# Kernel optimization log

Measured on AMD Instinct MI355X. Metric: run time of the kernel, lower is better.

Reference implementation:

```python
import jax, jax.numpy as jnp
import numpy as np

EPS = 1e-6

def _ln(x, g, b):
    mu = jnp.mean(x, -1, keepdims=True)
    var = jnp.mean((x - mu) ** 2, -1, keepdims=True)
    return (x - mu) / jnp.sqrt(var + EPS) * g + b

def _attn(q, k, v, nh, mask=None):
    B, Lq, H = q.shape
    Lk = k.shape[1]
    dh = H // nh
    q = q.reshape(B, Lq, nh, dh).transpose(0, 2, 1, 3)
    k = k.reshape(B, Lk, nh, dh).transpose(0, 2, 1, 3)
    v = v.reshape(B, Lk, nh, dh).transpose(0, 2, 1, 3)
    s = jnp.einsum('bhqd,bhkd->bhqk', q, k) * (1.0 / np.float32(np.sqrt(dh)))
    if mask is not None:
        s = jnp.where(mask, jnp.float32(-1e30), s)
    a = jax.nn.softmax(s, axis=-1)
    o = jnp.einsum('bhqk,bhkd->bhqd', a, v)
    return o.transpose(0, 2, 1, 3).reshape(B, Lq, H)

def _forward(byte_seq, patch_boundaries, emb, g_ln1_g, g_ln1_b, g_wqkv, g_bqkv, g_wo, g_bo,
             g_ln2_g, g_ln2_b, g_w1, g_b1, g_w2, g_b2, fn_g, fn_b,
             ca_ln_g, ca_ln_b, ca_wqkv, ca_bqkv, ca_wo, ca_bo, head_w, head_b,
             n_heads=16, ca_heads=8):
    B, S = byte_seq.shape
    P = patch_boundaries.shape[1]
    H = emb.shape[1]
    x = emb[byte_seq]  # [B,S,H] byte embeddings (local encoder)
    # ragged patch pooling: patch id of byte i = #boundaries <= i (BabylonIndex patches)
    pos = jnp.arange(S)
    pid = jax.vmap(lambda bd: jnp.searchsorted(bd, pos, side='right'))(patch_boundaries)
    pid = jnp.clip(pid, 0, P - 1)
    seg = lambda vals, ids: jax.ops.segment_sum(vals, ids, num_segments=P)
    sums = jax.vmap(seg)(x, pid)                                  # [B,P,H]
    cnts = jax.vmap(seg)(jnp.ones((B, S), x.dtype), pid)          # [B,P]
    patches = sums / jnp.maximum(cnts, 1.0)[..., None]            # mean-pooled patch reps
    causal = jnp.triu(jnp.ones((P, P), bool), 1)
    def layer(h, p):
        l1g, l1b, wqkv, bqkv, wo, bo, l2g, l2b, w1, b1, w2, b2 = p
        n = _ln(h, l1g, l1b)
        q, k, v = jnp.split(n @ wqkv + bqkv, 3, axis=-1)
        h = h + _attn(q, k, v, n_heads, causal) @ wo + bo
        n2 = _ln(h, l2g, l2b)
        h = h + jax.nn.gelu(n2 @ w1 + b1, approximate=False) @ w2 + b2
        return h, None
    patches, _ = jax.lax.scan(layer, patches, (g_ln1_g, g_ln1_b, g_wqkv, g_bqkv, g_wo, g_bo,
                                               g_ln2_g, g_ln2_b, g_w1, g_b1, g_w2, g_b2))
    patches = _ln(patches, fn_g, fn_b)  # GlobalLatentTransformer.final_norm
    # cross attention: byte queries attend to global patch representations
    qn = _ln(x, ca_ln_g, ca_ln_b)
    kvn = _ln(patches, ca_ln_g, ca_ln_b)
    q = qn @ ca_wqkv[:, :H] + ca_bqkv[:H]
    k = kvn @ ca_wqkv[:, H:2 * H] + ca_bqkv[H:2 * H]
    v = kvn @ ca_wqkv[:, 2 * H:] + ca_bqkv[2 * H:]
    h = x + _attn(q, k, v, ca_heads) @ ca_wo + ca_bo
    return h @ head_w + head_b  # [B,S,256] next-byte logits

def setup_inputs() -> dict:
    key = jax.random.key(0)
    ks = jax.random.split(key, 16)
    B, S, P, H, L, V = 2, 4096, 256, 1024, 4, 256
    std = 0.02
    d = {}
    d['byte_seq'] = jax.random.randint(ks[0], (B, S), 0, V, dtype=jnp.int32)
    d['patch_boundaries'] = jnp.sort(jax.random.randint(ks[1], (B, P), 1, S, dtype=jnp.int32), axis=-1)
    d['emb'] = jax.random.normal(ks[2], (V, H), jnp.float32) * std
    d['g_ln1_g'] = jnp.ones((L, H), jnp.float32)
    d['g_ln1_b'] = jnp.zeros((L, H), jnp.float32)
    d['g_wqkv'] = jax.random.normal(ks[3], (L, H, 3 * H), jnp.float32) * std
    d['g_bqkv'] = jnp.zeros((L, 3 * H), jnp.float32)
    d['g_wo'] = jax.random.normal(ks[4], (L, H, H), jnp.float32) * std
    d['g_bo'] = jnp.zeros((L, H), jnp.float32)
    d['g_ln2_g'] = jnp.ones((L, H), jnp.float32)
    d['g_ln2_b'] = jnp.zeros((L, H), jnp.float32)
    d['g_w1'] = jax.random.normal(ks[5], (L, H, 4 * H), jnp.float32) * std
    d['g_b1'] = jnp.zeros((L, 4 * H), jnp.float32)
    d['g_w2'] = jax.random.normal(ks[6], (L, 4 * H, H), jnp.float32) * std
    d['g_b2'] = jnp.zeros((L, H), jnp.float32)
    d['fn_g'] = jnp.ones((H,), jnp.float32)
    d['fn_b'] = jnp.zeros((H,), jnp.float32)
    d['ca_ln_g'] = jnp.ones((H,), jnp.float32)
    d['ca_ln_b'] = jnp.zeros((H,), jnp.float32)
    d['ca_wqkv'] = jax.random.normal(ks[7], (H, 3 * H), jnp.float32) * std
    d['ca_bqkv'] = jnp.zeros((3 * H,), jnp.float32)
    d['ca_wo'] = jax.random.normal(ks[8], (H, H), jnp.float32) * std
    d['ca_bo'] = jnp.zeros((H,), jnp.float32)
    d['head_w'] = jax.random.normal(ks[9], (H, V), jnp.float32) * std
    d['head_b'] = jnp.zeros((V,), jnp.float32)
    return d

def reference(byte_seq, patch_boundaries, emb, g_ln1_g, g_ln1_b, g_wqkv, g_bqkv, g_wo, g_bo,
              g_ln2_g, g_ln2_b, g_w1, g_b1, g_w2, g_b2, fn_g, fn_b,
              ca_ln_g, ca_ln_b, ca_wqkv, ca_bqkv, ca_wo, ca_bo, head_w, head_b):
    return _forward(byte_seq, patch_boundaries, emb, g_ln1_g, g_ln1_b, g_wqkv, g_bqkv, g_wo, g_bo,
                    g_ln2_g, g_ln2_b, g_w1, g_b1, g_w2, g_b2, fn_g, fn_b,
                    ca_ln_g, ca_ln_b, ca_wqkv, ca_bqkv, ca_wo, ca_bo, head_w, head_b)
```

## Files before the change

kernel.cpp:

```cpp
#include <hip/hip_runtime.h>
#include <hip/hip_bf16.h>
#include <math.h>

#define Hdim 1024
#define Bsz  2
#define Slen 4096
#define Pn   256
#define NLAY 4

typedef __attribute__((ext_vector_type(8))) __bf16 bfrag;
typedef __attribute__((ext_vector_type(4))) float  f32x4;

__device__ __forceinline__ float gelu_exact(float x) {
  return 0.5f * x * (1.0f + erff(x * 0.70710678118654752f));
}
__device__ __forceinline__ short f2b(float x) {
  __hip_bfloat16 h = __float2bfloat16(x);
  return *reinterpret_cast<short*>(&h);
}
__device__ __forceinline__ void gload16(const short* g, short* l) {
  __builtin_amdgcn_global_load_lds(
      (const __attribute__((address_space(1))) unsigned int*)g,
      (__attribute__((address_space(3))) unsigned int*)l, 16, 0, 0);
}
__device__ __forceinline__ void xcd_remap(int& bx, int& by) {
  int nwg = gridDim.x * gridDim.y;
  int bid = blockIdx.y * gridDim.x + blockIdx.x;
  int wg = (bid & 7) * (nwg >> 3) + (bid >> 3);
  bx = wg % gridDim.x;
  by = wg / gridDim.x;
}

__global__ void embed_ln_kernel(const int* __restrict__ seq, const float* __restrict__ emb,
                                const float* __restrict__ g, const float* __restrict__ bvec,
                                float* __restrict__ x, short* __restrict__ qn) {
  int row = blockIdx.x;
  int tid = threadIdx.x;
  int tok = seq[row];
  float4 v = *(const float4*)(emb + (size_t)tok * Hdim + tid * 4);
  *(float4*)(x + (size_t)row * Hdim + tid * 4) = v;
  float s  = v.x + v.y + v.z + v.w;
  float ss = v.x * v.x + v.y * v.y + v.z * v.z + v.w * v.w;
#pragma unroll
  for (int off = 32; off; off >>= 1) { s += __shfl_xor(s, off); ss += __shfl_xor(ss, off); }
  __shared__ float rs[4], rss[4];
  int wid = tid >> 6;
  if ((tid & 63) == 0) { rs[wid] = s; rss[wid] = ss; }
  __syncthreads();
  float tot  = rs[0] + rs[1] + rs[2] + rs[3];
  float tot2 = rss[0] + rss[1] + rss[2] + rss[3];
  float mu = tot * (1.0f / Hdim);
  float var = tot2 * (1.0f / Hdim) - mu * mu;
  float rstd = rsqrtf(var + 1e-6f);
  float4 gg = *(const float4*)(g + tid * 4);
  float4 bb = *(const float4*)(bvec + tid * 4);
  short4 o;
  o.x = f2b((v.x - mu) * rstd * gg.x + bb.x);
  o.y = f2b((v.y - mu) * rstd * gg.y + bb.y);
  o.z = f2b((v.z - mu) * rstd * gg.z + bb.z);
  o.w = f2b((v.w - mu) * rstd * gg.w + bb.w);
  *(short4*)(qn + (size_t)row * Hdim + tid * 4) = o;
}

__global__ void pid_kernel(const int* __restrict__ bounds, int* __restrict__ pid) {
  int i = blockIdx.x * 256 + threadIdx.x;
  int b = i >> 12;
  int s = i & (Slen - 1);
  const int* bd = bounds + b * Pn;
  int lo = 0, hi = Pn;
  while (lo < hi) { int m = (lo + hi) >> 1; if (bd[m] <= s) lo = m + 1; else hi = m; }
  pid[i] = min(lo, Pn - 1);
}

__global__ void pool_kernel(const float* __restrict__ x, const int* __restrict__ pid,
                            float* __restrict__ patches) {
  int bp = blockIdx.x;
  int b = bp >> 8;
  int p = bp & (Pn - 1);
  const int* pv = pid + b * Slen;
  int lo = 0, hi = Slen;
  while (lo < hi) { int m = (lo + hi) >> 1; if (pv[m] < p) lo = m + 1; else hi = m; }
  int start = lo;
  lo = 0; hi = Slen;
  while (lo < hi) { int m = (lo + hi) >> 1; if (pv[m] < p + 1) lo = m + 1; else hi = m; }
  int end = lo;
  int tid = threadIdx.x;
  float4 acc = {0.f, 0.f, 0.f, 0.f};
  for (int s = start; s < end; ++s) {
    float4 xv = *(const float4*)(x + ((size_t)(b * Slen + s)) * Hdim + tid * 4);
    acc.x += xv.x; acc.y += xv.y; acc.z += xv.z; acc.w += xv.w;
  }
  float cnt = (float)(end - start);
  float r = 1.0f / fmaxf(cnt, 1.0f);
  float4 o = {acc.x * r, acc.y * r, acc.z * r, acc.w * r};
  *(float4*)(patches + (size_t)bp * Hdim + tid * 4) = o;
}

template<int OBF>
__global__ void ln_kernel(const float* __restrict__ in, const float* __restrict__ g,
                          const float* __restrict__ bvec, void* __restrict__ outv) {
  int row = blockIdx.x;
  int tid = threadIdx.x;
  const float* xr = in + (size_t)row * Hdim;
  float4 v = *(const float4*)(xr + tid * 4);
  float s  = v.x + v.y + v.z + v.w;
  float ss = v.x * v.x + v.y * v.y + v.z * v.z + v.w * v.w;
#pragma unroll
  for (int off = 32; off; off >>= 1) { s += __shfl_xor(s, off); ss += __shfl_xor(ss, off); }
  __shared__ float rs[4], rss[4];
  int wid = tid >> 6;
  if ((tid & 63) == 0) { rs[wid] = s; rss[wid] = ss; }
  __syncthreads();
  float tot  = rs[0] + rs[1] + rs[2] + rs[3];
  float tot2 = rss[0] + rss[1] + rss[2] + rss[3];
  float mu = tot * (1.0f / Hdim);
  float var = tot2 * (1.0f / Hdim) - mu * mu;
  float rstd = rsqrtf(var + 1e-6f);
  float4 gg = *(const float4*)(g + tid * 4);
  float4 bb = *(const float4*)(bvec + tid * 4);
  float4 r;
  r.x = (v.x - mu) * rstd * gg.x + bb.x;
  r.y = (v.y - mu) * rstd * gg.y + bb.y;
  r.z = (v.z - mu) * rstd * gg.z + bb.z;
  r.w = (v.w - mu) * rstd * gg.w + bb.w;
  if (OBF) {
    short4 o; o.x = f2b(r.x); o.y = f2b(r.y); o.z = f2b(r.z); o.w = f2b(r.w);
    *(short4*)((short*)outv + (size_t)row * Hdim + tid * 4) = o;
  } else {
    *(float4*)((float*)outv + (size_t)row * Hdim + tid * 4) = r;
  }
}

__global__ void wconv_kernel(const float* __restrict__ in, short* __restrict__ out,
                             int ldin, int K, size_t in_lstride, size_t out_lstride) {
  int z = blockIdx.z;
  const float* src = in + (size_t)z * in_lstride;
  short* dst = out + (size_t)z * out_lstride;
  int n0 = blockIdx.x * 32, k0 = blockIdx.y * 32;
  int tx = threadIdx.x & 31, ty = threadIdx.x >> 5;
  __shared__ float t[32][33];
#pragma unroll
  for (int i = 0; i < 4; i++)
    t[ty + 8 * i][tx] = src[(size_t)(k0 + ty + 8 * i) * ldin + n0 + tx];
  __syncthreads();
#pragma unroll
  for (int i = 0; i < 4; i++)
    dst[(size_t)(n0 + ty + 8 * i) * K + k0 + tx] = f2b(t[tx][ty + 8 * i]);
}

__global__ void vt_kernel(const float* __restrict__ in, short* __restrict__ out) {
  int bh = blockIdx.z; int h = bh & 7; int b = bh >> 3;
  int kk0 = blockIdx.x * 32, d0 = blockIdx.y * 32;
  int tx = threadIdx.x & 31, ty = threadIdx.x >> 5;
  __shared__ float t[32][33];
  const float* src = in + (size_t)b * Pn * Hdim + h * 128;
#pragma unroll
  for (int i = 0; i < 4; i++)
    t[ty + 8 * i][tx] = src[(size_t)(kk0 + ty + 8 * i) * Hdim + d0 + tx];
  __syncthreads();
  short* dst = out + (size_t)bh * 128 * 256;
#pragma unroll
  for (int i = 0; i < 4; i++)
    dst[(size_t)(d0 + ty + 8 * i) * 256 + kk0 + tx] = f2b(t[tx][ty + 8 * i]);
}

__global__ void vtg_kernel(const short* __restrict__ qkvb, short* __restrict__ out) {
  int bh = blockIdx.z; int h = bh & 15; int b = bh >> 4;
  int kk0 = blockIdx.x * 32, d0 = blockIdx.y * 32;
  int tx = threadIdx.x & 31, ty = threadIdx.x >> 5;
  __shared__ short t[32][33];
  const short* src = qkvb + (size_t)b * Pn * 3072 + 2048 + h * 64;
#pragma unroll
  for (int i = 0; i < 4; i++)
    t[ty + 8 * i][tx] = src[(size_t)(kk0 + ty + 8 * i) * 3072 + d0 + tx];
  __syncthreads();
  short* dst = out + (size_t)bh * 64 * 256;
#pragma unroll
  for (int i = 0; i < 4; i++)
    dst[(size_t)(d0 + ty + 8 * i) * 256 + kk0 + tx] = t[tx][ty + 8 * i];
}

template<int EPI, int OBF, int SWZ>
__launch_bounds__(256)
__global__ void gemm_bf16(const short* __restrict__ A, const short* __restrict__ Bt,
                          const float* __restrict__ bias, const float* __restrict__ res,
                          void* __restrict__ Cv, int ldc, int K) {
  __shared__ short As[2][128 * 64];
  __shared__ short Bs[2][128 * 64];
  int tid = threadIdx.x;
  int bx = blockIdx.x, by = blockIdx.y;
  if (SWZ) xcd_remap(bx, by);
  int n0 = bx * 128, m0 = by * 128;
  int lr = tid >> 3;
  int lc = (((tid & 7) ^ (lr & 7)) * 8);
  int wid = tid >> 6, lane = tid & 63;
  int wm = (wid & 1) * 64, wn = (wid >> 1) * 64;
  int quad = lane >> 4, l16 = lane & 15;
  f32x4 acc[4][4];
#pragma unroll
  for (int i = 0; i < 4; i++)
#pragma unroll
    for (int j = 0; j < 4; j++) acc[i][j] = (f32x4){0.f, 0.f, 0.f, 0.f};

  const short* ga = A + (size_t)(m0 + lr) * K + lc;
  const short* gb = Bt + (size_t)(n0 + lr) * K + lc;
  short* la = &As[0][tid * 8];
  short* lb = &Bs[0][tid * 8];

#pragma unroll
  for (int r = 0; r < 4; r++) {
    gload16(ga + (size_t)(r * 32) * K, la + r * 2048);
    gload16(gb + (size_t)(r * 32) * K, lb + r * 2048);
  }
  asm volatile("s_waitcnt vmcnt(0)" ::: "memory");
  __builtin_amdgcn_s_barrier();

  int NT = K >> 6;
  for (int t = 0; t < NT; ++t) {
    int cur = t & 1;
    if (t + 1 < NT) {
      int nb = (cur ^ 1) * 8192;
      int k1 = (t + 1) << 6;
#pragma unroll
      for (int r = 0; r < 4; r++) {
        gload16(ga + (size_t)(r * 32) * K + k1, la + nb + r * 2048);
        gload16(gb + (size_t)(r * 32) * K + k1, lb + nb + r * 2048);
      }
    }
#pragma unroll
    for (int kk = 0; kk < 2; kk++) {
      bfrag af[4], bfv[4];
#pragma unroll
      for (int mi = 0; mi < 4; mi++) {
        int row = wm + mi * 16 + l16;
        af[mi] = *reinterpret_cast<const bfrag*>(
            &As[cur][row * 64 + (((kk * 4 + quad) ^ (row & 7)) * 8)]);
      }
#pragma unroll
      for (int ni = 0; ni < 4; ni++) {
        int row = wn + ni * 16 + l16;
        bfv[ni] = *reinterpret_cast<const bfrag*>(
            &Bs[cur][row * 64 + (((kk * 4 + quad) ^ (row & 7)) * 8)]);
      }
#pragma unroll
      for (int mi = 0; mi < 4; mi++)
#pragma unroll
        for (int ni = 0; ni < 4; ni++)
          acc[mi][ni] = __builtin_amdgcn_mfma_f32_16x16x32_bf16(af[mi], bfv[ni], acc[mi][ni], 0, 0, 0);
    }
    asm volatile("s_waitcnt vmcnt(0)" ::: "memory");
    __builtin_amdgcn_s_barrier();
  }

#pragma unroll
  for (int mi = 0; mi < 4; mi++)
#pragma unroll
    for (int ni = 0; ni < 4; ni++) {
      int c = n0 + wn + ni * 16 + l16;
      float bsv = bias[c];
#pragma unroll
      for (int reg = 0; reg < 4; reg++) {
        int r = m0 + wm + mi * 16 + quad * 4 + reg;
        float v = acc[mi][ni][reg] + bsv;
        if (EPI == 1) v = gelu_exact(v);
        if (EPI == 2) v += res[(size_t)r * ldc + c];
        if (OBF) ((short*)Cv)[(size_t)r * ldc + c] = f2b(v);
        else     ((float*)Cv)[(size_t)r * ldc + c] = v;
      }
    }
}

template<int EPI, int OBF, int SWZ>
__launch_bounds__(256)
__global__ void gemm_bf16_64(const short* __restrict__ A, const short* __restrict__ Bt,
                             const float* __restrict__ bias, const float* __restrict__ res,
                             void* __restrict__ Cv, int ldc, int K) {
  __shared__ short As[2][64 * 64];
  __shared__ short Bs[2][64 * 64];
  int tid = threadIdx.x;
  int bx = blockIdx.x, by = blockIdx.y;
  if (SWZ) xcd_remap(bx, by);
  int n0 = bx * 64, m0 = by * 64;
  int lr = tid >> 3;
  int lc = (((tid & 7) ^ (lr & 7)) * 8);
  int wid = tid >> 6, lane = tid & 63;
  int wm = (wid & 1) * 32, wn = (wid >> 1) * 32;
  int quad = lane >> 4, l16 = lane & 15;
  f32x4 acc[2][2];
#pragma unroll
  for (int i = 0; i < 2; i++)
#pragma unroll
    for (int j = 0; j < 2; j++) acc[i][j] = (f32x4){0.f, 0.f, 0.f, 0.f};

  const short* ga = A + (size_t)(m0 + lr) * K + lc;
  const short* gb = Bt + (size_t)(n0 + lr) * K + lc;
  short* la = &As[0][tid * 8];
  short* lb = &Bs[0][tid * 8];

#pragma unroll
  for (int r = 0; r < 2; r++) {
    gload16(ga + (size_t)(r * 32) * K, la + r * 2048);
    gload16(gb + (size_t)(r * 32) * K, lb + r * 2048);
  }
  asm volatile("s_waitcnt vmcnt(0)" ::: "memory");
  __builtin_amdgcn_s_barrier();

  int NT = K >> 6;
  for (int t = 0; t < NT; ++t) {
    int cur = t & 1;
    if (t + 1 < NT) {
      int nb = (cur ^ 1) * 4096;
      int k1 = (t + 1) << 6;
#pragma unroll
      for (int r = 0; r < 2; r++) {
        gload16(ga + (size_t)(r * 32) * K + k1, la + nb + r * 2048);
        gload16(gb + (size_t)(r * 32) * K + k1, lb + nb + r * 2048);
      }
    }
#pragma unroll
    for (int kk = 0; kk < 2; kk++) {
      bfrag af[2], bfv[2];
#pragma unroll
      for (int mi = 0; mi < 2; mi++) {
        int row = wm + mi * 16 + l16;
        af[mi] = *reinterpret_cast<const bfrag*>(
            &As[cur][row * 64 + (((kk * 4 + quad) ^ (row & 7)) * 8)]);
      }
#pragma unroll
      for (int ni = 0; ni < 2; ni++) {
        int row = wn + ni * 16 + l16;
        bfv[ni] = *reinterpret_cast<const bfrag*>(
            &Bs[cur][row * 64 + (((kk * 4 + quad) ^ (row & 7)) * 8)]);
      }
#pragma unroll
      for (int mi = 0; mi < 2; mi++)
#pragma unroll
        for (int ni = 0; ni < 2; ni++)
          acc[mi][ni] = __builtin_amdgcn_mfma_f32_16x16x32_bf16(af[mi], bfv[ni], acc[mi][ni], 0, 0, 0);
    }
    asm volatile("s_waitcnt vmcnt(0)" ::: "memory");
    __builtin_amdgcn_s_barrier();
  }

#pragma unroll
  for (int mi = 0; mi < 2; mi++)
#pragma unroll
    for (int ni = 0; ni < 2; ni++) {
      int c = n0 + wn + ni * 16 + l16;
      float bsv = bias[c];
#pragma unroll
      for (int reg = 0; reg < 4; reg++) {
        int r = m0 + wm + mi * 16 + quad * 4 + reg;
        float v = acc[mi][ni][reg] + bsv;
        if (EPI == 1) v = gelu_exact(v);
        if (EPI == 2) v += res[(size_t)r * ldc + c];
        if (OBF) ((short*)Cv)[(size_t)r * ldc + c] = f2b(v);
        else     ((float*)Cv)[(size_t)r * ldc + c] = v;
      }
    }
}

__launch_bounds__(256)
__global__ void gemm_splitk(const short* __restrict__ A, const short* __restrict__ Bt,
                            float* __restrict__ part, int K, int Ks) {
  __shared__ short As[2][64 * 64];
  __shared__ short Bs[2][64 * 64];
  int tid = threadIdx.x;
  int n0 = blockIdx.x * 64, m0 = blockIdx.y * 64, s = blockIdx.z;
  int kbase = s * Ks;
  int lr = tid >> 3;
  int lc = (((tid & 7) ^ (lr & 7)) * 8);
  int wid = tid >> 6, lane = tid & 63;
  int wm = (wid & 1) * 32, wn = (wid >> 1) * 32;
  int quad = lane >> 4, l16 = lane & 15;
  f32x4 acc[2][2];
#pragma unroll
  for (int i = 0; i < 2; i++)
#pragma unroll
    for (int j = 0; j < 2; j++) acc[i][j] = (f32x4){0.f, 0.f, 0.f, 0.f};

  const short* ga = A + (size_t)(m0 + lr) * K + kbase + lc;
  const short* gb = Bt + (size_t)(n0 + lr) * K + kbase + lc;
  short* la = &As[0][tid * 8];
  short* lb = &Bs[0][tid * 8];

#pragma unroll
  for (int r = 0; r < 2; r++) {
    gload16(ga + (size_t)(r * 32) * K, la + r * 2048);
    gload16(gb + (size_t)(r * 32) * K, lb + r * 2048);
  }
  asm volatile("s_waitcnt vmcnt(0)" ::: "memory");
  __builtin_amdgcn_s_barrier();

  int NT = Ks >> 6;
  for (int t = 0; t < NT; ++t) {
    int cur = t & 1;
    if (t + 1 < NT) {
      int nb = (cur ^ 1) * 4096;
      int k1 = (t + 1) << 6;
#pragma unroll
      for (int r = 0; r < 2; r++) {
        gload16(ga + (size_t)(r * 32) * K + k1, la + nb + r * 2048);
        gload16(gb + (size_t)(r * 32) * K + k1, lb + nb + r * 2048);
      }
    }
#pragma unroll
    for (int kk = 0; kk < 2; kk++) {
      bfrag af[2], bfv[2];
#pragma unroll
      for (int mi = 0; mi < 2; mi++) {
        int row = wm + mi * 16 + l16;
        af[mi] = *reinterpret_cast<const bfrag*>(
            &As[cur][row * 64 + (((kk * 4 + quad) ^ (row & 7)) * 8)]);
      }
#pragma unroll
      for (int ni = 0; ni < 2; ni++) {
        int row = wn + ni * 16 + l16;
        bfv[ni] = *reinterpret_cast<const bfrag*>(
            &Bs[cur][row * 64 + (((kk * 4 + quad) ^ (row & 7)) * 8)]);
      }
#pragma unroll
      for (int mi = 0; mi < 2; mi++)
#pragma unroll
        for (int ni = 0; ni < 2; ni++)
          acc[mi][ni] = __builtin_amdgcn_mfma_f32_16x16x32_bf16(af[mi], bfv[ni], acc[mi][ni], 0, 0, 0);
    }
    asm volatile("s_waitcnt vmcnt(0)" ::: "memory");
    __builtin_amdgcn_s_barrier();
  }

#pragma unroll
  for (int mi = 0; mi < 2; mi++)
#pragma unroll
    for (int ni = 0; ni < 2; ni++) {
      int c = n0 + wn + ni * 16 + l16;
#pragma unroll
      for (int reg = 0; reg < 4; reg++) {
        int r = m0 + wm + mi * 16 + quad * 4 + reg;
        part[(size_t)s * 524288 + (size_t)r * 1024 + c] = acc[mi][ni][reg];
      }
    }
}

__global__ void w2red_kernel(const float* __restrict__ part, const float* __restrict__ bias,
                             float* __restrict__ patches) {
  int i = (blockIdx.x * 256 + threadIdx.x) * 4;
  float4 v = *(const float4*)(part + i);
#pragma unroll
  for (int s = 1; s < 4; s++) {
    float4 p = *(const float4*)(part + (size_t)s * 524288 + i);
    v.x += p.x; v.y += p.y; v.z += p.z; v.w += p.w;
  }
  int c = i & 1023;
  float4 bv = *(const float4*)(bias + c);
  float4 rv = *(const float4*)(patches + i);
  v.x += bv.x + rv.x; v.y += bv.y + rv.y; v.z += bv.z + rv.z; v.w += bv.w + rv.w;
  *(float4*)(patches + i) = v;
}

__launch_bounds__(256)
__global__ void attn_global3(const short* __restrict__ qkvb, const short* __restrict__ vtg,
                             short* __restrict__ outp) {
  int qt = blockIdx.x;
  int bh = blockIdx.y; int h = bh & 15, b = bh >> 4;
  int tid = threadIdx.x;
  int wid = tid >> 6, lane = tid & 63;
  int quad = lane >> 4, l16 = lane & 15;
  int q0 = qt * 64 + wid * 16;
  __shared__ short KV[64 * 72];
  __shared__ short Pl[4][16][264];
  const short* qrow = qkvb + ((size_t)(b * Pn + q0 + l16)) * 3072 + h * 64 + quad * 8;
  bfrag qf[2];
#pragma unroll
  for (int kd = 0; kd < 2; kd++) qf[kd] = *(const bfrag*)(qrow + kd * 32);
  f32x4 sacc[16];
#pragma unroll
  for (int n = 0; n < 16; n++) sacc[n] = (f32x4){0.f, 0.f, 0.f, 0.f};
  int cr = tid >> 2, cc = (tid & 3) * 16;
#pragma unroll
  for (int kc = 0; kc < 4; kc++) {
    if (kc <= qt) {
      const short* ksrc = qkvb + ((size_t)(b * Pn + kc * 64 + cr)) * 3072 + 1024 + h * 64 + cc;
      int4 v0 = *(const int4*)(ksrc);
      int4 v1 = *(const int4*)(ksrc + 8);
      __syncthreads();
      *(int4*)&KV[cr * 72 + cc] = v0;
      *(int4*)&KV[cr * 72 + cc + 8] = v1;
      __syncthreads();
#pragma unroll
      for (int n = 0; n < 4; n++)
#pragma unroll
        for (int kd = 0; kd < 2; kd++) {
          bfrag kf = *(const bfrag*)&KV[(n * 16 + l16) * 72 + kd * 32 + quad * 8];
          sacc[kc * 4 + n] = __builtin_amdgcn_mfma_f32_16x16x32_bf16(qf[kd], kf, sacc[kc * 4 + n], 0, 0, 0);
        }
    }
  }
  int nfr = (qt + 1) * 4;
  const float scale = 0.125f;
  float mx[4] = {-1e30f, -1e30f, -1e30f, -1e30f};
#pragma unroll
  for (int n = 0; n < 16; n++) {
    if (n < nfr) {
      int col = n * 16 + l16;
#pragma unroll
      for (int r = 0; r < 4; r++)
        if (col <= q0 + quad * 4 + r) mx[r] = fmaxf(mx[r], sacc[n][r]);
    }
  }
#pragma unroll
  for (int off = 1; off < 16; off <<= 1)
#pragma unroll
    for (int r = 0; r < 4; r++) mx[r] = fmaxf(mx[r], __shfl_xor(mx[r], off));
  float ls[4] = {0.f, 0.f, 0.f, 0.f};
#pragma unroll
  for (int n = 0; n < 16; n++) {
    if (n < nfr) {
      int col = n * 16 + l16;
#pragma unroll
      for (int r = 0; r < 4; r++) {
        float p = (col <= q0 + quad * 4 + r) ? __expf((sacc[n][r] - mx[r]) * scale) : 0.f;
        Pl[wid][quad * 4 + r][col] = f2b(p);
        ls[r] += p;
      }
    }
  }
#pragma unroll
  for (int off = 1; off < 16; off <<= 1)
#pragma unroll
    for (int r = 0; r < 4; r++) ls[r] += __shfl_xor(ls[r], off);
  float rl[4];
#pragma unroll
  for (int r = 0; r < 4; r++) rl[r] = 1.0f / ls[r];

  f32x4 oacc[4];
#pragma unroll
  for (int n = 0; n < 4; n++) oacc[n] = (f32x4){0.f, 0.f, 0.f, 0.f};
#pragma unroll
  for (int kc = 0; kc < 4; kc++) {
    if (kc <= qt) {
      const short* vsrc = vtg + (size_t)bh * 64 * 256 + cr * 256 + kc * 64 + cc;
      int4 v0 = *(const int4*)(vsrc);
      int4 v1 = *(const int4*)(vsrc + 8);
      __syncthreads();
      *(int4*)&KV[cr * 72 + cc] = v0;
      *(int4*)&KV[cr * 72 + cc + 8] = v1;
      __syncthreads();
#pragma unroll
      for (int kk = 0; kk < 2; kk++) {
        bfrag pa = *(const bfrag*)&Pl[wid][l16][kc * 64 + kk * 32 + quad * 8];
#pragma unroll
        for (int n = 0; n < 4; n++) {
          bfrag vf = *(const bfrag*)&KV[(n * 16 + l16) * 72 + kk * 32 + quad * 8];
          oacc[n] = __builtin_amdgcn_mfma_f32_16x16x32_bf16(pa, vf, oacc[n], 0, 0, 0);
        }
      }
    }
  }
#pragma unroll
  for (int n = 0; n < 4; n++)
#pragma unroll
    for (int r = 0; r < 4; r++)
      outp[(size_t)(b * Pn + q0 + quad * 4 + r) * Hdim + h * 64 + n * 16 + l16] = f2b(oacc[n][r] * rl[r]);
}

__launch_bounds__(256)
__global__ void attn_cross4(const short* __restrict__ q, const short* __restrict__ k,
                            const short* __restrict__ vt, short* __restrict__ outp) {
  int bh = blockIdx.y; int h = bh & 7, b = bh >> 3;
  int tid = threadIdx.x;
  int wid = tid >> 6, lane = tid & 63;
  int quad = lane >> 4, l16 = lane & 15;
  int q0 = blockIdx.x * 64 + wid * 16;
  __shared__ short KV[9216];
  __shared__ short Pl[4][16][264];
  const short* qrow = q + ((size_t)(b * Slen + q0 + l16)) * Hdim + h * 128 + quad * 8;
  bfrag qf[4];
#pragma unroll
  for (int kd = 0; kd < 4; kd++) qf[kd] = *(const bfrag*)(qrow + kd * 32);
  f32x4 sacc[16];
#pragma unroll
  for (int n = 0; n < 16; n++) sacc[n] = (f32x4){0.f, 0.f, 0.f, 0.f};

  int cr4 = tid >> 2, cc4 = (tid & 3) * 32;
#pragma unroll
  for (int kc = 0; kc < 4; kc++) {
    const short* ksrc = k + ((size_t)(b * Pn + kc * 64 + cr4)) * Hdim + h * 128 + cc4;
    int4 v0 = *(const int4*)(ksrc);
    int4 v1 = *(const int4*)(ksrc + 8);
    int4 v2 = *(const int4*)(ksrc + 16);
    int4 v3 = *(const int4*)(ksrc + 24);
    __syncthreads();
    *(int4*)&KV[cr4 * 136 + cc4]      = v0;
    *(int4*)&KV[cr4 * 136 + cc4 + 8]  = v1;
    *(int4*)&KV[cr4 * 136 + cc4 + 16] = v2;
    *(int4*)&KV[cr4 * 136 + cc4 + 24] = v3;
    __syncthreads();
#pragma unroll
    for (int n = 0; n < 4; n++)
#pragma unroll
      for (int kd = 0; kd < 4; kd++) {
        bfrag kf = *(const bfrag*)&KV[(n * 16 + l16) * 136 + kd * 32 + quad * 8];
        sacc[kc * 4 + n] = __builtin_amdgcn_mfma_f32_16x16x32_bf16(qf[kd], kf, sacc[kc * 4 + n], 0, 0, 0);
      }
  }

  const float scale = 0.088388347648318447f;
  float mx[4] = {-1e30f, -1e30f, -1e30f, -1e30f};
#pragma unroll
  for (int n = 0; n < 16; n++)
#pragma unroll
    for (int r = 0; r < 4; r++) mx[r] = fmaxf(mx[r], sacc[n][r]);
#pragma unroll
  for (int off = 1; off < 16; off <<= 1)
#pragma unroll
    for (int r = 0; r < 4; r++) mx[r] = fmaxf(mx[r], __shfl_xor(mx[r], off));
  float ls[4] = {0.f, 0.f, 0.f, 0.f};
#pragma unroll
  for (int n = 0; n < 16; n++)
#pragma unroll
    for (int r = 0; r < 4; r++) {
      float p = __expf((sacc[n][r] - mx[r]) * scale);
      Pl[wid][quad * 4 + r][n * 16 + l16] = f2b(p);
      ls[r] += p;
    }
#pragma unroll
  for (int off = 1; off < 16; off <<= 1)
#pragma unroll
    for (int r = 0; r < 4; r++) ls[r] += __shfl_xor(ls[r], off);
  float rl[4];
#pragma unroll
  for (int r = 0; r < 4; r++) rl[r] = 1.0f / ls[r];

  f32x4 oacc[8];
#pragma unroll
  for (int n = 0; n < 8; n++) oacc[n] = (f32x4){0.f, 0.f, 0.f, 0.f};
  int cr2 = tid >> 1, cc2 = (tid & 1) * 32;
#pragma unroll
  for (int kc = 0; kc < 4; kc++) {
    const short* vsrc = vt + (size_t)bh * 32768 + cr2 * 256 + kc * 64 + cc2;
    int4 v0 = *(const int4*)(vsrc);
    int4 v1 = *(const int4*)(vsrc + 8);
    int4 v2 = *(const int4*)(vsrc + 16);
    int4 v3 = *(const int4*)(vsrc + 24);
    __syncthreads();
    *(int4*)&KV[cr2 * 72 + cc2]      = v0;
    *(int4*)&KV[cr2 * 72 + cc2 + 8]  = v1;
    *(int4*)&KV[cr2 * 72 + cc2 + 16] = v2;
    *(int4*)&KV[cr2 * 72 + cc2 + 24] = v3;
    __syncthreads();
#pragma unroll
    for (int kk = 0; kk < 2; kk++) {
      bfrag pa = *(const bfrag*)&Pl[wid][l16][kc * 64 + kk * 32 + quad * 8];
#pragma unroll
      for (int n = 0; n < 8; n++) {
        bfrag vf = *(const bfrag*)&KV[(n * 16 + l16) * 72 + kk * 32 + quad * 8];
        oacc[n] = __builtin_amdgcn_mfma_f32_16x16x32_bf16(pa, vf, oacc[n], 0, 0, 0);
      }
    }
  }
#pragma unroll
  for (int n = 0; n < 8; n++)
#pragma unroll
    for (int r = 0; r < 4; r++)
      outp[(size_t)(b * Slen + q0 + quad * 4 + r) * Hdim + h * 128 + n * 16 + l16] = f2b(oacc[n][r] * rl[r]);
}

extern "C" void kernel_launch(void* const* d_in, const int* in_sizes, int n_in,
                              void* d_out, int out_size, void* d_ws, size_t ws_size,
                              hipStream_t stream) {
  const int*   byte_seq = (const int*)d_in[0];
  const int*   pbound   = (const int*)d_in[1];
  const float* emb      = (const float*)d_in[2];
  const float* g_ln1_g  = (const float*)d_in[3];
  const float* g_ln1_b  = (const float*)d_in[4];
  const float* g_wqkv   = (const float*)d_in[5];
  const float* g_bqkv   = (const float*)d_in[6];
  const float* g_wo     = (const float*)d_in[7];
  const float* g_bo     = (const float*)d_in[8];
  const float* g_ln2_g  = (const float*)d_in[9];
  const float* g_ln2_b  = (const float*)d_in[10];
  const float* g_w1     = (const float*)d_in[11];
  const float* g_b1     = (const float*)d_in[12];
  const float* g_w2     = (const float*)d_in[13];
  const float* g_b2     = (const float*)d_in[14];
  const float* fn_g     = (const float*)d_in[15];
  const float* fn_b     = (const float*)d_in[16];
  const float* ca_ln_g  = (const float*)d_in[17];
  const float* ca_ln_b  = (const float*)d_in[18];
  const float* ca_wqkv  = (const float*)d_in[19];
  const float* ca_bqkv  = (const float*)d_in[20];
  const float* ca_wo    = (const float*)d_in[21];
  const float* ca_bo    = (const float*)d_in[22];
  const float* head_w   = (const float*)d_in[23];
  const float* head_b   = (const float*)d_in[24];
  float* out = (float*)d_out;

  float* x       = (float*)d_ws;
  float* patches = x + 8388608;
  float* vbuf    = patches + 524288;
  float* w2part  = vbuf + 524288;
  int*   pid     = (int*)(w2part + 2097152);
  short* nbuf    = (short*)(pid + 8192);
  short* attn_o  = nbuf + 524288;
  short* mid     = attn_o + 524288;
  short* qn      = mid + 2097152;
  short* qb      = qn + 8388608;
  short* xb      = qb + 8388608;
  short* kb      = xb + 8388608;
  short* vt      = kb + 524288;
  short* qkvb    = vt + 524288;
  short* vtg     = qkvb + 1572864;
  short* wqkv_t  = vtg + 524288;
  short* wo_t    = wqkv_t + 12582912;
  short* w1_t    = wo_t + 4194304;
  short* w2_t    = w1_t + 16777216;
  short* caq_t   = w2_t + 16777216;
  short* cak_t   = caq_t + 1048576;
  short* cav_t   = cak_t + 1048576;
  short* cawo_t  = cav_t + 1048576;
  short* head_t  = cawo_t + 1048576;
  short* caout   = qn;

  embed_ln_kernel<<<Bsz * Slen, 256, 0, stream>>>(byte_seq, emb, ca_ln_g, ca_ln_b, x, qn);
  pid_kernel<<<(Bsz * Slen) / 256, 256, 0, stream>>>(pbound, pid);
  pool_kernel<<<Bsz * Pn, 256, 0, stream>>>(x, pid, patches);

  wconv_kernel<<<dim3(96, 32, 4), 256, 0, stream>>>(g_wqkv, wqkv_t, 3072, 1024, 3145728, 3145728);
  wconv_kernel<<<dim3(32, 32, 4), 256, 0, stream>>>(g_wo, wo_t, 1024, 1024, 1048576, 1048576);
  wconv_kernel<<<dim3(128, 32, 4), 256, 0, stream>>>(g_w1, w1_t, 4096, 1024, 4194304, 4194304);
  wconv_kernel<<<dim3(32, 128, 4), 256, 0, stream>>>(g_w2, w2_t, 1024, 4096, 4194304, 4194304);
  wconv_kernel<<<dim3(32, 32, 3), 256, 0, stream>>>(ca_wqkv, caq_t, 3072, 1024, 1024, 1048576);
  wconv_kernel<<<dim3(32, 32, 1), 256, 0, stream>>>(ca_wo, cawo_t, 1024, 1024, 0, 0);
  wconv_kernel<<<dim3(8, 32, 1), 256, 0, stream>>>(head_w, head_t, 256, 1024, 0, 0);

  for (int l = 0; l < NLAY; ++l) {
    ln_kernel<1><<<Bsz * Pn, 256, 0, stream>>>(patches, g_ln1_g + l * Hdim, g_ln1_b + l * Hdim, nbuf);
    gemm_bf16_64<0, 1, 0><<<dim3(48, 8), 256, 0, stream>>>(
        nbuf, wqkv_t + (size_t)l * 3145728, g_bqkv + l * 3072, nullptr, qkvb, 3072, 1024);
    vtg_kernel<<<dim3(8, 2, 32), 256, 0, stream>>>(qkvb, vtg);
    attn_global3<<<dim3(4, 32), 256, 0, stream>>>(qkvb, vtg, attn_o);
    gemm_bf16_64<2, 0, 0><<<dim3(16, 8), 256, 0, stream>>>(
        attn_o, wo_t + (size_t)l * 1048576, g_bo + l * Hdim, patches, patches, 1024, 1024);
    ln_kernel<1><<<Bsz * Pn, 256, 0, stream>>>(patches, g_ln2_g + l * Hdim, g_ln2_b + l * Hdim, nbuf);
    gemm_bf16_64<1, 1, 0><<<dim3(64, 8), 256, 0, stream>>>(
        nbuf, w1_t + (size_t)l * 4194304, g_b1 + l * 4096, nullptr, mid, 4096, 1024);
    gemm_splitk<<<dim3(16, 8, 4), 256, 0, stream>>>(
        mid, w2_t + (size_t)l * 4194304, w2part, 4096, 1024);
    w2red_kernel<<<512, 256, 0, stream>>>(w2part, g_b2 + l * Hdim, patches);
  }

  ln_kernel<0><<<Bsz * Pn, 256, 0, stream>>>(patches, fn_g, fn_b, patches);
  ln_kernel<1><<<Bsz * Pn, 256, 0, stream>>>(patches, ca_ln_g, ca_ln_b, nbuf);

  gemm_bf16_64<0, 1, 0><<<dim3(16, 8), 256, 0, stream>>>(
      nbuf, cak_t, ca_bqkv + 1024, nullptr, kb, 1024, 1024);
  gemm_bf16_64<0, 0, 0><<<dim3(16, 8), 256, 0, stream>>>(
      nbuf, cav_t, ca_bqkv + 2048, nullptr, vbuf, 1024, 1024);
  vt_kernel<<<dim3(8, 4, 16), 256, 0, stream>>>(vbuf, vt);

  gemm_bf16<0, 1, 1><<<dim3(8, 64), 256, 0, stream>>>(
      qn, caq_t, ca_bqkv, nullptr, qb, 1024, 1024);

  attn_cross4<<<dim3(64, 16), 256, 0, stream>>>(qb, kb, vt, caout);

  gemm_bf16<2, 1, 1><<<dim3(8, 64), 256, 0, stream>>>(
      caout, cawo_t, ca_bo, x, xb, 1024, 1024);

  gemm_bf16_64<0, 0, 1><<<dim3(4, 128), 256, 0, stream>>>(
      xb, head_t, head_b, nullptr, out, 256, 1024);
}
```

Before: 771.5 us.

## Double-buffer cross-attention K/V staging with async global-to-LDS loads and XOR swizzle

Rewrites the cross-attention kernel's K and V staging. It now uses direct global-to-LDS loads into two buffers, so the next chunk loads while MFMAs run on the current one, and the V prefetch overlaps the softmax. Padded LDS rows are replaced by an XOR swizzle to avoid bank conflicts, and half the __syncthreads pairs become single barriers with explicit vmcnt waits. The price is more complex synchronisation that depends on the waitcnt ordering being correct. Only this one kernel out of many in the forward pass is affected.

```diff
diff --git a/kernel.cpp b/kernel.cpp
--- a/kernel.cpp
+++ b/kernel.cpp
@@ -565,44 +565,74 @@
 }
 
 __launch_bounds__(256)
-__global__ void attn_cross4(const short* __restrict__ q, const short* __restrict__ k,
+__global__ void attn_cross5(const short* __restrict__ q, const short* __restrict__ k,
                             const short* __restrict__ vt, short* __restrict__ outp) {
   int bh = blockIdx.y; int h = bh & 7, b = bh >> 3;
   int tid = threadIdx.x;
   int wid = tid >> 6, lane = tid & 63;
   int quad = lane >> 4, l16 = lane & 15;
   int q0 = blockIdx.x * 64 + wid * 16;
-  __shared__ short KV[9216];
+  __shared__ short KV[2][8192];
   __shared__ short Pl[4][16][264];
+
   const short* qrow = q + ((size_t)(b * Slen + q0 + l16)) * Hdim + h * 128 + quad * 8;
   bfrag qf[4];
 #pragma unroll
   for (int kd = 0; kd < 4; kd++) qf[kd] = *(const bfrag*)(qrow + kd * 32);
+
+  const short* kbase = k + (size_t)(b * Pn) * Hdim + h * 128;
+  const short* vbase = vt + (size_t)bh * 32768;
+  int krow = tid >> 4;
+  int vrow = tid >> 3;
+  int swzK = (tid & 15) ^ (krow & 7);
+  int swzV = (tid & 7) ^ (vrow & 7);
+  int s3 = l16 & 7;
+
   f32x4 sacc[16];
 #pragma unroll
   for (int n = 0; n < 16; n++) sacc[n] = (f32x4){0.f, 0.f, 0.f, 0.f};
 
-  int cr4 = tid >> 2, cc4 = (tid & 3) * 32;
+  {
+    const short* src = kbase + (size_t)krow * Hdim + swzK * 8;
+    short* dst = &KV[0][tid * 8];
+#pragma unroll
+    for (int r = 0; r < 4; r++)
+      gload16(src + (size_t)(r * 16) * Hdim, dst + r * 2048);
+  }
+  asm volatile("s_waitcnt vmcnt(0)" ::: "memory");
+  __builtin_amdgcn_s_barrier();
+
 #pragma unroll
   for (int kc = 0; kc < 4; kc++) {
-    const short* ksrc = k + ((size_t)(b * Pn + kc * 64 + cr4)) * Hdim + h * 128 + cc4;
-    int4 v0 = *(const int4*)(ksrc);
-    int4 v1 = *(const int4*)(ksrc + 8);
-    int4 v2 = *(const int4*)(ksrc + 16);
-    int4 v3 = *(const int4*)(ksrc + 24);
-    __syncthreads();
-    *(int4*)&KV[cr4 * 136 + cc4]      = v0;
-    *(int4*)&KV[cr4 * 136 + cc4 + 8]  = v1;
-    *(int4*)&KV[cr4 * 136 + cc4 + 16] = v2;
-    *(int4*)&KV[cr4 * 136 + cc4 + 24] = v3;
-    __syncthreads();
-#pragma unroll
-    for (int n = 0; n < 4; n++)
+    if (kc < 3) {
+      const short* src = kbase + (size_t)((kc + 1) * 64 + krow) * Hdim + swzK * 8;
+      short* dst = &KV[(kc + 1) & 1][tid * 8];
+#pragma unroll
+      for (int r = 0; r < 4; r++)
+        gload16(src + (size_t)(r * 16) * Hdim, dst + r * 2048);
+    }
+    const short* kv = KV[kc & 1];
+#pragma unroll
+    for (int n = 0; n < 4; n++) {
+      int roff = (n * 16 + l16) * 128;
 #pragma unroll
       for (int kd = 0; kd < 4; kd++) {
-        bfrag kf = *(const bfrag*)&KV[(n * 16 + l16) * 136 + kd * 32 + quad * 8];
+        bfrag kf = *(const bfrag*)&kv[roff + (((kd * 4 + quad) ^ s3) * 8)];
         sacc[kc * 4 + n] = __builtin_amdgcn_mfma_f32_16x16x32_bf16(qf[kd], kf, sacc[kc * 4 + n], 0, 0, 0);
       }
+    }
+    asm volatile("s_waitcnt vmcnt(0)" ::: "memory");
+    __builtin_amdgcn_s_barrier();
+  }
+
+  {
+    const short* src0 = vbase + (size_t)vrow * 256 + swzV * 8;
+    const short* src1 = src0 + 64;
+#pragma unroll
+    for (int r = 0; r < 4; r++) {
+      gload16(src0 + (size_t)(r * 32) * 256, &KV[0][tid * 8 + r * 2048]);
+      gload16(src1 + (size_t)(r * 32) * 256, &KV[1][tid * 8 + r * 2048]);
+    }
   }
 
   const float scale = 0.088388347648318447f;
@@ -632,33 +662,51 @@
 #pragma unroll
   for (int r = 0; r < 4; r++) rl[r] = 1.0f / ls[r];
 
+  asm volatile("s_waitcnt vmcnt(0)" ::: "memory");
+  __builtin_amdgcn_s_barrier();
+
   f32x4 oacc[8];
 #pragma unroll
   for (int n = 0; n < 8; n++) oacc[n] = (f32x4){0.f, 0.f, 0.f, 0.f};
-  int cr2 = tid >> 1, cc2 = (tid & 1) * 32;
-#pragma unroll
-  for (int kc = 0; kc < 4; kc++) {
-    const short* vsrc = vt + (size_t)bh * 32768 + cr2 * 256 + kc * 64 + cc2;
-    int4 v0 = *(const int4*)(vsrc);
-    int4 v1 = *(const int4*)(vsrc + 8);
-    int4 v2 = *(const int4*)(vsrc + 16);
-    int4 v3 = *(const int4*)(vsrc + 24);
-    __syncthreads();
-    *(int4*)&KV[cr2 * 72 + cc2]      = v0;
-    *(int4*)&KV[cr2 * 72 + cc2 + 8]  = v1;
-    *(int4*)&KV[cr2 * 72 + cc2 + 16] = v2;
-    *(int4*)&KV[cr2 * 72 + cc2 + 24] = v3;
-    __syncthreads();
-#pragma unroll
-    for (int kk = 0; kk < 2; kk++) {
-      bfrag pa = *(const bfrag*)&Pl[wid][l16][kc * 64 + kk * 32 + quad * 8];
-#pragma unroll
-      for (int n = 0; n < 8; n++) {
-        bfrag vf = *(const bfrag*)&KV[(n * 16 + l16) * 72 + kk * 32 + quad * 8];
-        oacc[n] = __builtin_amdgcn_mfma_f32_16x16x32_bf16(pa, vf, oacc[n], 0, 0, 0);
-      }
-    }
-  }
+
+#define PVCHUNK(KC, BUF)                                                              \
+  do {                                                                                \
+    const short* vv = (BUF);                                                          \
+    _Pragma("unroll")                                                                 \
+    for (int kk = 0; kk < 2; kk++) {                                                  \
+      bfrag pa = *(const bfrag*)&Pl[wid][l16][(KC) * 64 + kk * 32 + quad * 8];        \
+      _Pragma("unroll")                                                               \
+      for (int n = 0; n < 8; n++) {                                                   \
+        bfrag vf = *(const bfrag*)&vv[(n * 16 + l16) * 64 + (((kk * 4 + quad) ^ s3) * 8)]; \
+        oacc[n] = __builtin_amdgcn_mfma_f32_16x16x32_bf16(pa, vf, oacc[n], 0, 0, 0);  \
+      }                                                                               \
+    }                                                                                 \
+  } while (0)
+
+#define STAGEV(KC, BUF)                                                               \
+  do {                                                                                \
+    const short* src = vbase + (size_t)vrow * 256 + (KC) * 64 + swzV * 8;             \
+    short* dst = (BUF) + tid * 8;                                                     \
+    _Pragma("unroll")                                                                 \
+    for (int r = 0; r < 4; r++)                                                       \
+      gload16(src + (size_t)(r * 32) * 256, dst + r * 2048);                          \
+  } while (0)
+
+  PVCHUNK(0, KV[0]);
+  __builtin_amdgcn_s_barrier();
+  STAGEV(2, KV[0]);
+  PVCHUNK(1, KV[1]);
+  __builtin_amdgcn_s_barrier();
+  STAGEV(3, KV[1]);
+  asm volatile("s_waitcnt vmcnt(4)" ::: "memory");
+  __builtin_amdgcn_s_barrier();
+  PVCHUNK(2, KV[0]);
+  asm volatile("s_waitcnt vmcnt(0)" ::: "memory");
+  __builtin_amdgcn_s_barrier();
+  PVCHUNK(3, KV[1]);
+#undef PVCHUNK
+#undef STAGEV
+
 #pragma unroll
   for (int n = 0; n < 8; n++)
 #pragma unroll
@@ -762,7 +810,7 @@
   gemm_bf16<0, 1, 1><<<dim3(8, 64), 256, 0, stream>>>(
       qn, caq_t, ca_bqkv, nullptr, qb, 1024, 1024);
 
-  attn_cross4<<<dim3(64, 16), 256, 0, stream>>>(qb, kb, vt, caout);
+  attn_cross5<<<dim3(64, 16), 256, 0, stream>>>(qb, kb, vt, caout);
 
   gemm_bf16<2, 1, 1><<<dim3(8, 64), 256, 0, stream>>>(
       caout, cawo_t, ca_bo, x, xb, 1024, 1024);
```

Measured after the change: 768.7 us. No clear change (-0.4%).
